# Performance work log

Hardware: AMD Instinct MI355X
Metric: run time of the kernel (lower is better)

## Reference

```python
import jax, jax.numpy as jnp
import numpy as np
from jax import lax

CIN, COUT, NCLS = 512, 256, 1
B, H, W = 4, 64, 64
EPS = 1e-5


def conv1x1(x, w):
    # x: [B,I,H,W], w: [O,I]
    return jnp.einsum('oi,bihw->bohw', w, x)


def conv3x3(x, w):
    # x: [B,I,H,W], w: [O,I,3,3], padding=1
    return lax.conv_general_dilated(x, w, (1, 1), 'SAME',
                                    dimension_numbers=('NCHW', 'OIHW', 'NCHW'))


def bn_relu(x, g, b):
    # training-mode BatchNorm2d (biased var over B,H,W) + ReLU
    mean = jnp.mean(x, axis=(0, 2, 3), keepdims=True)
    var = jnp.var(x, axis=(0, 2, 3), keepdims=True)
    xn = (x - mean) * lax.rsqrt(var + EPS)
    return jax.nn.relu(xn * g[None, :, None, None] + b[None, :, None, None])


def attention(xf, yf, wq, wk, wv, gamma):
    # cross-attn when yf != xf, self-attn when yf is xf; no 1/sqrt(d) scaling (faithful)
    Bb, C, Hh, Ww = xf.shape
    N = Hh * Ww
    q = conv1x1(xf, wq).reshape(Bb, C, N)
    k = conv1x1(yf, wk).reshape(Bb, C, N)
    v = conv1x1(yf, wv).reshape(Bb, C, N)
    att = jax.nn.softmax(jnp.einsum('bcn,bcm->bnm', q, k), axis=-1)  # [B,N,N]
    out = jnp.einsum('bcm,bnm->bcn', v, att).reshape(Bb, C, Hh, Ww)  # v @ att^T
    return gamma * out + xf


def setup_inputs() -> dict:
    key = jax.random.key(0)
    ks = jax.random.split(key, 16)
    Cs = COUT + 2

    def w(k, shape, fan_in):
        return jax.random.normal(k, shape, dtype=jnp.float32) / np.sqrt(fan_in)

    return {
        'x': jax.random.normal(ks[0], (B, CIN, H, W), dtype=jnp.float32),
        'y': jax.random.normal(ks[1], (B, CIN, H, W), dtype=jnp.float32),
        'flow': jax.random.normal(ks[2], (B, 2, H, W), dtype=jnp.float32),
        'w1x1': w(ks[3], (COUT, CIN), CIN),
        'b1x1': jnp.zeros((COUT,), dtype=jnp.float32),
        'ca_wq': w(ks[4], (COUT, COUT), COUT),
        'ca_wk': w(ks[5], (COUT, COUT), COUT),
        'ca_wv': w(ks[6], (COUT, COUT), COUT),
        'ca_gamma': jnp.full((1,), 0.1, dtype=jnp.float32),
        'cbr1_w': w(ks[7], (COUT, COUT, 3, 3), COUT * 9),
        'bn1_g': jnp.ones((COUT,), dtype=jnp.float32),
        'bn1_b': jnp.zeros((COUT,), dtype=jnp.float32),
        'sa_wq': w(ks[8], (Cs, Cs), Cs),
        'sa_wk': w(ks[9], (Cs, Cs), Cs),
        'sa_wv': w(ks[10], (Cs, Cs), Cs),
        'sa_gamma': jnp.full((1,), 0.1, dtype=jnp.float32),
        'cbr2_w': w(ks[11], (COUT, Cs, 3, 3), Cs * 9),
        'bn2_g': jnp.ones((COUT,), dtype=jnp.float32),
        'bn2_b': jnp.zeros((COUT,), dtype=jnp.float32),
        'pred_w': w(ks[12], (NCLS, COUT), COUT),
        'pred_b': jnp.zeros((NCLS,), dtype=jnp.float32),
    }


def reference(x, y, flow, w1x1, b1x1, ca_wq, ca_wk, ca_wv, ca_gamma,
              cbr1_w, bn1_g, bn1_b, sa_wq, sa_wk, sa_wv, sa_gamma,
              cbr2_w, bn2_g, bn2_b, pred_w, pred_b):
    xb = conv1x1(x, w1x1) + b1x1[None, :, None, None]
    yb = conv1x1(y, w1x1) + b1x1[None, :, None, None]
    t = attention(xb, yb, ca_wq, ca_wk, ca_wv, ca_gamma)
    cross_out = bn_relu(conv3x3(t, cbr1_w), bn1_g, bn1_b)
    cat = jnp.concatenate([cross_out, flow], axis=1)  # [B, COUT+2, H, W]
    t = attention(cat, cat, sa_wq, sa_wk, sa_wv, sa_gamma)
    t = bn_relu(conv3x3(t, cbr2_w), bn2_g, bn2_b)
    out = conv1x1(t, pred_w) + pred_b[None, :, None, None]
    return out
```

## Files before the change

### kernel.cpp

```cpp
#include <hip/hip_runtime.h>
#include <hip/hip_bf16.h>
#include <math.h>


#define NPIX 4096
#define NB   4

typedef __attribute__((ext_vector_type(8))) short short8v;
typedef __attribute__((ext_vector_type(4))) float float4v;

__device__ __forceinline__ short f2bs(float f) {
  __hip_bfloat16 h = __float2bfloat16(f);
  short r; __builtin_memcpy(&r, &h, 2); return r;
}

__global__ __launch_bounds__(256) void transp_kernel(
    const float* __restrict__ X, __hip_bfloat16* __restrict__ XT)
{
  const int i0 = blockIdx.x * 64, n0 = blockIdx.y * 64, b = blockIdx.z;
  const int tid = threadIdx.x;
  __shared__ float Ls[64][68];
#pragma unroll
  for (int it = 0; it < 4; ++it) {
    int ir = it * 16 + (tid >> 4);
    int nc = (tid & 15) * 4;
    float4 v = *(const float4*)(X + ((size_t)b * 512 + i0 + ir) * NPIX + n0 + nc);
    *(float4*)(&Ls[ir][nc]) = v;
  }
  __syncthreads();
#pragma unroll
  for (int ot = 0; ot < 2; ++ot) {
    int n = ot * 32 + (tid >> 3);
    int ig = tid & 7;
    short8v o;
#pragma unroll
    for (int j = 0; j < 8; ++j) o[j] = f2bs(Ls[8 * ig + j][n]);
    *(short8v*)(XT + ((size_t)b * NPIX + n0 + n) * 512 + i0 + 8 * ig) = o;
  }
}

__global__ void wprep_kernel(const float* __restrict__ Win,
                             __hip_bfloat16* __restrict__ Wout,
                             int Or, int Ir, int Op, int Ip)
{
  size_t total = (size_t)Op * Ip;
  for (size_t e = (size_t)blockIdx.x * 256 + threadIdx.x; e < total;
       e += (size_t)gridDim.x * 256) {
    int i = (int)(e % Ip);
    int o = (int)(e / Ip);
    float v = (o < Or && i < Ir) ? Win[(size_t)o * Ir + i] : 0.f;
    Wout[e] = __float2bfloat16(v);
  }
}

__global__ void wtransbf_kernel(const float* __restrict__ Win,
                                __hip_bfloat16* __restrict__ Wout,
                                int O, int Ir, int Ip)
{
  size_t total = (size_t)9 * O * Ip;
  for (size_t e = (size_t)blockIdx.x * 256 + threadIdx.x; e < total;
       e += (size_t)gridDim.x * 256) {
    int i = (int)(e % Ip);
    size_t r = e / Ip;
    int o = (int)(r % O);
    int dydx = (int)(r / O);
    float v = (i < Ir) ? Win[((size_t)o * Ir + i) * 9 + dydx] : 0.f;
    Wout[e] = __float2bfloat16(v);
  }
}

template<int OMODE>
__global__ __launch_bounds__(256, 3) void gemm3_kernel(
    const __hip_bfloat16* __restrict__ X, const __hip_bfloat16* __restrict__ Wb,
    const float* __restrict__ Bias, float* __restrict__ Yf,
    __hip_bfloat16* __restrict__ Yb, int Ip, int O)
{
  const int n0 = blockIdx.x * 64, o0 = blockIdx.y * 64, b = blockIdx.z;
  const int tid = threadIdx.x, wv = tid >> 6, lane = tid & 63;
  const int lg = lane >> 4, lr = lane & 15;
  __shared__ __align__(16) __hip_bfloat16 Xs[64 * 32];
  __shared__ __align__(16) __hip_bfloat16 Wsh[64 * 32];

  const int nn = tid >> 2, ig = tid & 3;
  const __hip_bfloat16* xrow = X + ((size_t)b * NPIX + n0 + nn) * Ip;
  const __hip_bfloat16* wrow = Wb + (size_t)(o0 + nn) * Ip;
  const int sw = 8 * (ig ^ (nn & 3));

  float4v acc[4];
#pragma unroll
  for (int f = 0; f < 4; ++f) acc[f] = (float4v){0.f, 0.f, 0.f, 0.f};

  const int nch = Ip >> 5;
  short8v xr_ = *(const short8v*)(xrow + sw);
  short8v wr_ = *(const short8v*)(wrow + sw);

  for (int ci = 0; ci < nch; ++ci) {
    __syncthreads();
    *(short8v*)(Xs  + nn * 32 + ig * 8) = xr_;
    *(short8v*)(Wsh + nn * 32 + ig * 8) = wr_;
    __syncthreads();
    if (ci + 1 < nch) {
      xr_ = *(const short8v*)(xrow + (ci + 1) * 32 + sw);
      wr_ = *(const short8v*)(wrow + (ci + 1) * 32 + sw);
    }
    if (OMODE < 2) {
      int ar = 16 * wv + lr;
      short8v a = *(const short8v*)(Xs + ar * 32 + 8 * (lg ^ (ar & 3)));
#pragma unroll
      for (int of = 0; of < 4; ++of) {
        int br = 16 * of + lr;
        short8v bb = *(const short8v*)(Wsh + br * 32 + 8 * (lg ^ (br & 3)));
        acc[of] = __builtin_amdgcn_mfma_f32_16x16x32_bf16(a, bb, acc[of], 0, 0, 0);
      }
    } else {
      int ar = 16 * wv + lr;
      short8v a = *(const short8v*)(Wsh + ar * 32 + 8 * (lg ^ (ar & 3)));
#pragma unroll
      for (int nf = 0; nf < 4; ++nf) {
        int br = 16 * nf + lr;
        short8v bb = *(const short8v*)(Xs + br * 32 + 8 * (lg ^ (br & 3)));
        acc[nf] = __builtin_amdgcn_mfma_f32_16x16x32_bf16(a, bb, acc[nf], 0, 0, 0);
      }
    }
  }

  if (OMODE < 2) {
#pragma unroll
    for (int r = 0; r < 4; ++r) {
      size_t row = (size_t)b * NPIX + n0 + 16 * wv + 4 * lg + r;
#pragma unroll
      for (int of = 0; of < 4; ++of) {
        int o = o0 + 16 * of + lr;
        if (o < O) {
          float v = acc[of][r] + (Bias ? Bias[o] : 0.f);
          if (OMODE == 0) Yf[row * O + o] = v;
          Yb[row * O + o] = __float2bfloat16(v);
        }
      }
    }
  } else {
#pragma unroll
    for (int r = 0; r < 4; ++r) {
      int c = o0 + 16 * wv + 4 * lg + r;
      if (c < O) {
#pragma unroll
        for (int nf = 0; nf < 4; ++nf) {
          int n = n0 + 16 * nf + lr;
          Yb[((size_t)b * O + c) * NPIX + n] = __float2bfloat16(acc[nf][r]);
        }
      }
    }
  }
}

template<int C>
__global__ __launch_bounds__(256, 2) void flash3_kernel(
    const __hip_bfloat16* __restrict__ Q, const __hip_bfloat16* __restrict__ K,
    const __hip_bfloat16* __restrict__ V,
    __hip_bfloat16* __restrict__ Opart, float* __restrict__ ml)
{
  constexpr int N = NPIX;
  constexpr int NC32 = C / 32;
  constexpr int NCF  = C / 16;
  constexpr int SPR  = C / 8;
  constexpr int NST  = C / 32;
  const int n0 = blockIdx.x * 64;
  const int split = blockIdx.y;
  const int b = blockIdx.z;
  const int tid = threadIdx.x, w = tid >> 6, lane = tid & 63;
  const int lg = lane >> 4, lr = lane & 15;

  __shared__ __align__(16) __hip_bfloat16 Ks[64 * C];
  __shared__ __align__(16) __hip_bfloat16 Vs[C * 64];
  __shared__ __align__(16) __hip_bfloat16 Ps[4][64][16];

  short8v qf[NC32];
  {
    const __hip_bfloat16* qp = Q + ((size_t)b * N + n0 + 16 * w + lr) * C + 8 * lg;
#pragma unroll
    for (int ks = 0; ks < NC32; ++ks) qf[ks] = *(const short8v*)(qp + 32 * ks);
  }

  float4v oacc[NCF];
#pragma unroll
  for (int f = 0; f < NCF; ++f) oacc[f] = (float4v){0.f, 0.f, 0.f, 0.f};
  float mrun[4], lrun[4];
#pragma unroll
  for (int r = 0; r < 4; ++r) { mrun[r] = -INFINITY; lrun[r] = 0.f; }

  const __hip_bfloat16* Kb = K + (size_t)b * N * C;
  const __hip_bfloat16* Vb = V + (size_t)b * C * N;
  const int m0 = split * (N / 2);

  short8v kreg[NST], vreg[NST];
#pragma unroll
  for (int i = 0; i < NST; ++i) {
    int s = tid + i * 256;
    int row = s / SPR, c8i = s % SPR;
    kreg[i] = *(const short8v*)(Kb + (size_t)(m0 + row) * C + 8 * (c8i ^ (row & 3)));
  }
#pragma unroll
  for (int i = 0; i < NST; ++i) {
    int s = tid + i * 256;
    int c = s >> 3, m8i = s & 7;
    vreg[i] = *(const short8v*)(Vb + (size_t)c * N + m0 + 8 * (m8i ^ (c & 3)));
  }

  for (int t = 0; t < 32; ++t) {
    __syncthreads();
#pragma unroll
    for (int i = 0; i < NST; ++i) {
      int s = tid + i * 256;
      *(short8v*)(Ks + s * 8) = kreg[i];
      *(short8v*)(Vs + s * 8) = vreg[i];
    }
    __syncthreads();
    if (t < 31) {
      const int mn = m0 + (t + 1) * 64;
#pragma unroll
      for (int i = 0; i < NST; ++i) {
        int s = tid + i * 256;
        int row = s / SPR, c8i = s % SPR;
        kreg[i] = *(const short8v*)(Kb + (size_t)(mn + row) * C + 8 * (c8i ^ (row & 3)));
      }
#pragma unroll
      for (int i = 0; i < NST; ++i) {
        int s = tid + i * 256;
        int c = s >> 3, m8i = s & 7;
        vreg[i] = *(const short8v*)(Vb + (size_t)c * N + mn + 8 * (m8i ^ (c & 3)));
      }
    }
    float4v sacc[4];
#pragma unroll
    for (int mf = 0; mf < 4; ++mf) sacc[mf] = (float4v){0.f, 0.f, 0.f, 0.f};
#pragma unroll
    for (int ks = 0; ks < NC32; ++ks)
#pragma unroll
      for (int mf = 0; mf < 4; ++mf) {
        int m = 16 * mf + lr;
        short8v k8 = *(const short8v*)(Ks + m * C + 32 * ks + 8 * (lg ^ (m & 3)));
        sacc[mf] = __builtin_amdgcn_mfma_f32_16x16x32_bf16(qf[ks], k8, sacc[mf], 0, 0, 0);
      }
    float scal[4];
#pragma unroll
    for (int r = 0; r < 4; ++r) {
      float pm = fmaxf(fmaxf(sacc[0][r], sacc[1][r]), fmaxf(sacc[2][r], sacc[3][r]));
#pragma unroll
      for (int off = 1; off < 16; off <<= 1) pm = fmaxf(pm, __shfl_xor(pm, off));
      float mnew = fmaxf(mrun[r], pm);
      float sc = __expf(mrun[r] - mnew);
      mrun[r] = mnew;
      float rs = 0.f, p[4];
#pragma unroll
      for (int mf = 0; mf < 4; ++mf) { p[mf] = __expf(sacc[mf][r] - mnew); rs += p[mf]; }
#pragma unroll
      for (int mf = 0; mf < 4; ++mf)
        Ps[mf][16 * w + 4 * lg + r][lr] = __float2bfloat16(p[mf]);
#pragma unroll
      for (int off = 1; off < 16; off <<= 1) rs += __shfl_xor(rs, off);
      lrun[r] = lrun[r] * sc + rs;
      scal[r] = sc;
    }
#pragma unroll
    for (int f = 0; f < NCF; ++f)
#pragma unroll
      for (int r = 0; r < 4; ++r) oacc[f][r] *= scal[r];

    asm volatile("s_waitcnt lgkmcnt(0)" ::: "memory");

    short8v pa0 = *(const short8v*)(&Ps[lg >> 1][16 * w + lr][8 * (lg & 1)]);
    short8v pa1 = *(const short8v*)(&Ps[2 + (lg >> 1)][16 * w + lr][8 * (lg & 1)]);
#pragma unroll
    for (int cf = 0; cf < NCF; ++cf) {
      int c = 16 * cf + lr;
      const __hip_bfloat16* vb = Vs + c * 64;
      short8v v0 = *(const short8v*)(vb + 8 * (lg ^ (c & 3)));
      short8v v1 = *(const short8v*)(vb + 32 + 8 * (lg ^ (c & 3)));
      oacc[cf] = __builtin_amdgcn_mfma_f32_16x16x32_bf16(pa0, v0, oacc[cf], 0, 0, 0);
      oacc[cf] = __builtin_amdgcn_mfma_f32_16x16x32_bf16(pa1, v1, oacc[cf], 0, 0, 0);
    }
  }
  const size_t rbase = (size_t)(split * NB + b) * N;
#pragma unroll
  for (int r = 0; r < 4; ++r) {
    int n = n0 + 16 * w + 4 * lg + r;
    if (lr == 0) { ml[(rbase + n) * 2] = mrun[r]; ml[(rbase + n) * 2 + 1] = lrun[r]; }
#pragma unroll
    for (int cf = 0; cf < NCF; ++cf)
      Opart[(rbase + n) * C + 16 * cf + lr] = __float2bfloat16(oacc[cf][r]);
  }
}

template<int C>
__global__ __launch_bounds__(256) void merge3_kernel(
    const __hip_bfloat16* __restrict__ Op, const float* __restrict__ ml,
    const float* __restrict__ R, const float* __restrict__ gamma_p,
    __hip_bfloat16* __restrict__ T)
{
  const size_t row = blockIdx.x;
  const size_t row1 = row + (size_t)NB * NPIX;
  float m0 = ml[row * 2],  l0 = ml[row * 2 + 1];
  float m1 = ml[row1 * 2], l1 = ml[row1 * 2 + 1];
  float m = fmaxf(m0, m1);
  float e0 = __expf(m0 - m), e1 = __expf(m1 - m);
  float rinv = gamma_p[0] / (l0 * e0 + l1 * e1);
  for (int c = threadIdx.x; c < C; c += 256) {
    float o = __bfloat162float(Op[row * C + c]) * e0 +
              __bfloat162float(Op[row1 * C + c]) * e1;
    T[row * C + c] = __float2bfloat16(o * rinv + R[row * C + c]);
  }
}

template<int IC>
__global__ __launch_bounds__(256, 2) void conv3_kernel(
    const __hip_bfloat16* __restrict__ X, const __hip_bfloat16* __restrict__ W2,
    float* __restrict__ Y)
{
  constexpr int NCH = IC / 32;
  constexpr int XP = 66 * 32;
  const int h = blockIdx.x, o0 = blockIdx.y * 64, b = blockIdx.z;
  const int tid = threadIdx.x, wv = tid >> 6, lane = tid & 63;
  const int lg = lane >> 4, lr = lane & 15;

  __shared__ __align__(16) __hip_bfloat16 Ws[9 * 64 * 32];
  __shared__ __align__(16) __hip_bfloat16 X3[3 * XP];

  for (int e = tid; e < 192; e += 256) {
    int p = e / 64, rr = (e >> 5) & 1, i = e & 31;
    X3[p * XP + (rr ? 65 * 32 : 0) + i] = __float2bfloat16(0.f);
  }

  float4v acc[4];
#pragma unroll
  for (int f = 0; f < 4; ++f) acc[f] = (float4v){0.f, 0.f, 0.f, 0.f};

  short8v xreg[3], wreg[9];
#define LOADX(CI)                                                              \
  _Pragma("unroll")                                                            \
  for (int j = 0; j < 3; ++j) {                                                \
    int s = tid + j * 256;                                                     \
    int dy = s >> 8, ww = (s >> 2) & 63, ig = s & 3;                           \
    int hs = h + dy - 1;                                                       \
    if (hs >= 0 && hs < 64)                                                    \
      xreg[j] = *(const short8v*)(X + ((size_t)b * NPIX + hs * 64 + ww) * IC + \
                                  (CI) * 32 + 8 * (ig ^ ((ww + 1) & 3)));      \
    else                                                                       \
      xreg[j] = (short8v){0, 0, 0, 0, 0, 0, 0, 0};                             \
  }
#define LOADW(CI)                                                              \
  _Pragma("unroll")                                                            \
  for (int j = 0; j < 9; ++j) {                                                \
    int s = tid + j * 256;                                                     \
    int dydx = s >> 8, oo = (s >> 2) & 63, ig = s & 3;                         \
    wreg[j] = *(const short8v*)(W2 + ((size_t)(dydx * 256 + o0 + oo)) * IC +   \
                                (CI) * 32 + 8 * (ig ^ (oo & 3)));              \
  }
  LOADX(0); LOADW(0);

  for (int ci = 0; ci < NCH; ++ci) {
    __syncthreads();
#pragma unroll
    for (int j = 0; j < 3; ++j) {
      int s = tid + j * 256;
      int dy = s >> 8, ww = (s >> 2) & 63, ig = s & 3;
      *(short8v*)(X3 + dy * XP + (ww + 1) * 32 + ig * 8) = xreg[j];
    }
#pragma unroll
    for (int j = 0; j < 9; ++j) {
      int s = tid + j * 256;
      *(short8v*)(Ws + s * 8) = wreg[j];
    }
    __syncthreads();
    if (ci + 1 < NCH) { LOADX(ci + 1); LOADW(ci + 1); }
#pragma unroll
    for (int dy = 0; dy < 3; ++dy)
#pragma unroll
      for (int dx = 0; dx < 3; ++dx) {
        int rs_ = 16 * wv + lr + dx;
        short8v a = *(const short8v*)(X3 + dy * XP + rs_ * 32 + 8 * (lg ^ (rs_ & 3)));
#pragma unroll
        for (int of = 0; of < 4; ++of) {
          int br = 16 * of + lr;
          short8v bb = *(const short8v*)(Ws + (dy * 3 + dx) * 2048 + br * 32 +
                                         8 * (lg ^ (br & 3)));
          acc[of] = __builtin_amdgcn_mfma_f32_16x16x32_bf16(a, bb, acc[of], 0, 0, 0);
        }
      }
  }
#pragma unroll
  for (int r = 0; r < 4; ++r) {
    size_t row = (size_t)b * NPIX + h * 64 + 16 * wv + 4 * lg + r;
#pragma unroll
    for (int of = 0; of < 4; ++of)
      Y[row * 256 + o0 + 16 * of + lr] = acc[of][r];
  }
#undef LOADX
#undef LOADW
}

__global__ __launch_bounds__(256) void stats1_kernel(
    const float* __restrict__ X, float* __restrict__ Part)
{
  const int o0 = (blockIdx.x & 3) * 64;
  const int rc = blockIdx.x >> 2;
  const int tid = threadIdx.x;
  const int o = o0 + (tid & 63), rq = tid >> 6;
  float s = 0.f, sq = 0.f;
  for (int rr = rq; rr < 256; rr += 4) {
    float v = X[(size_t)(rc * 256 + rr) * 256 + o];
    s += v; sq += v * v;
  }
  __shared__ float rs[256], rq2[256];
  rs[tid] = s; rq2[tid] = sq;
  __syncthreads();
  if (tid < 64) {
    s  = rs[tid] + rs[tid + 64] + rs[tid + 128] + rs[tid + 192];
    sq = rq2[tid] + rq2[tid + 64] + rq2[tid + 128] + rq2[tid + 192];
    Part[(o0 + tid) * 128 + rc * 2]     = s;
    Part[(o0 + tid) * 128 + rc * 2 + 1] = sq;
  }
}

__global__ __launch_bounds__(256) void stats2_kernel(
    const float* __restrict__ Part, float* __restrict__ Mean, float* __restrict__ Rstd)
{
  const int o = threadIdx.x;
  float s = 0.f, sq = 0.f;
  for (int rc = 0; rc < 64; ++rc) {
    s += Part[o * 128 + rc * 2];
    sq += Part[o * 128 + rc * 2 + 1];
  }
  float mean = s / 16384.f;
  float var = sq / 16384.f - mean * mean;
  Mean[o] = mean;
  Rstd[o] = 1.f / sqrtf(var + 1e-5f);
}

__global__ __launch_bounds__(320) void bnapply1_kernel(
    const float* __restrict__ X, const float* __restrict__ Flow,
    const float* __restrict__ Mean, const float* __restrict__ Rstd,
    const float* __restrict__ G, const float* __restrict__ Bt,
    float* __restrict__ CatF, __hip_bfloat16* __restrict__ CatB)
{
  const size_t row = blockIdx.x;
  const int t = threadIdx.x;
  if (t >= 288) return;
  float val;
  if (t < 256) {
    float v = X[row * 256 + t];
    val = fmaxf((v - Mean[t]) * Rstd[t] * G[t] + Bt[t], 0.f);
  } else if (t < 258) {
    int b = (int)(row >> 12), n = (int)(row & 4095);
    val = Flow[((size_t)(b * 2 + (t - 256)) << 12) + n];
  } else val = 0.f;
  CatF[row * 288 + t] = val;
  CatB[row * 288 + t] = __float2bfloat16(val);
}

__global__ __launch_bounds__(256) void bnapply2_kernel(
    float* X, const float* __restrict__ Mean, const float* __restrict__ Rstd,
    const float* __restrict__ G, const float* __restrict__ Bt)
{
  const size_t idx = (size_t)blockIdx.x * 256 + threadIdx.x;
  const int t = threadIdx.x;
  float v = X[idx];
  X[idx] = fmaxf((v - Mean[t]) * Rstd[t] * G[t] + Bt[t], 0.f);
}

__global__ __launch_bounds__(256) void pred3_kernel(
    const float* __restrict__ X, const float* __restrict__ Wp,
    const float* __restrict__ Bp, float* __restrict__ Out)
{
  const int wv = threadIdx.x >> 6, lane = threadIdx.x & 63;
  const size_t row = (size_t)blockIdx.x * 4 + wv;
  const float* xr = X + row * 256;
  float acc = 0.f;
#pragma unroll
  for (int cc = 0; cc < 4; ++cc) acc = fmaf(xr[cc * 64 + lane], Wp[cc * 64 + lane], acc);
#pragma unroll
  for (int off = 1; off < 64; off <<= 1) acc += __shfl_xor(acc, off);
  if (lane == 0) Out[row] = acc + Bp[0];
}

extern "C" void kernel_launch(void* const* d_in, const int* in_sizes, int n_in,
                              void* d_out, int out_size, void* d_ws, size_t ws_size,
                              hipStream_t stream)
{
  (void)in_sizes; (void)n_in; (void)out_size; (void)ws_size;
  const float* x      = (const float*)d_in[0];
  const float* y      = (const float*)d_in[1];
  const float* flow   = (const float*)d_in[2];
  const float* w1x1   = (const float*)d_in[3];
  const float* b1x1   = (const float*)d_in[4];
  const float* ca_wq  = (const float*)d_in[5];
  const float* ca_wk  = (const float*)d_in[6];
  const float* ca_wv  = (const float*)d_in[7];
  const float* ca_g   = (const float*)d_in[8];
  const float* cbr1_w = (const float*)d_in[9];
  const float* bn1_g  = (const float*)d_in[10];
  const float* bn1_b  = (const float*)d_in[11];
  const float* sa_wq  = (const float*)d_in[12];
  const float* sa_wk  = (const float*)d_in[13];
  const float* sa_wv  = (const float*)d_in[14];
  const float* sa_g   = (const float*)d_in[15];
  const float* cbr2_w = (const float*)d_in[16];
  const float* bn2_g  = (const float*)d_in[17];
  const float* bn2_b  = (const float*)d_in[18];
  const float* pred_w = (const float*)d_in[19];
  const float* pred_b = (const float*)d_in[20];
  float* out = (float*)d_out;

  const size_t FSZ = (size_t)NB * NPIX * 288;
  const size_t SSZ = FSZ / 2;
  float* ws = (float*)d_ws;
  float* F0 = ws;
  float* F1 = ws + FSZ;
  float* F2 = ws + 2 * FSZ;
  float* Sb = ws + 3 * FSZ;
  __hip_bfloat16* S0 = (__hip_bfloat16*)(Sb);
  __hip_bfloat16* S1 = (__hip_bfloat16*)(Sb + SSZ);
  __hip_bfloat16* S2 = (__hip_bfloat16*)(Sb + 2 * SSZ);
  __hip_bfloat16* S3 = (__hip_bfloat16*)(Sb + 3 * SSZ);
  __hip_bfloat16* S4 = (__hip_bfloat16*)(Sb + 4 * SSZ);
  float* Wr = Sb + 5 * SSZ;
  __hip_bfloat16* w1bf  = (__hip_bfloat16*)Wr;
  __hip_bfloat16* caqb  = w1bf + (size_t)256 * 512;
  __hip_bfloat16* cakb  = caqb + (size_t)256 * 256;
  __hip_bfloat16* cavb  = cakb + (size_t)256 * 256;
  __hip_bfloat16* saqb  = cavb + (size_t)256 * 256;
  __hip_bfloat16* sakb  = saqb + (size_t)320 * 288;
  __hip_bfloat16* savb  = sakb + (size_t)320 * 288;
  __hip_bfloat16* w2abf = savb + (size_t)320 * 288;
  __hip_bfloat16* w2bbf = w2abf + (size_t)9 * 256 * 256;
  float* Part = (float*)(w2bbf + (size_t)9 * 256 * 288);
  float* Mean = Part + 32768;
  float* Rstd = Mean + 256;
  float* Mlb  = Rstd + 256;

  __hip_bfloat16* xT = (__hip_bfloat16*)F0;
  __hip_bfloat16* yT = (__hip_bfloat16*)F1;
  __hip_bfloat16* Op = (__hip_bfloat16*)F0;

  dim3 blk(256);

  wprep_kernel<<<dim3(256), blk, 0, stream>>>(w1x1, w1bf, 256, 512, 256, 512);
  wprep_kernel<<<dim3(256), blk, 0, stream>>>(ca_wq, caqb, 256, 256, 256, 256);
  wprep_kernel<<<dim3(256), blk, 0, stream>>>(ca_wk, cakb, 256, 256, 256, 256);
  wprep_kernel<<<dim3(256), blk, 0, stream>>>(ca_wv, cavb, 256, 256, 256, 256);
  wprep_kernel<<<dim3(256), blk, 0, stream>>>(sa_wq, saqb, 258, 258, 320, 288);
  wprep_kernel<<<dim3(256), blk, 0, stream>>>(sa_wk, sakb, 258, 258, 320, 288);
  wprep_kernel<<<dim3(256), blk, 0, stream>>>(sa_wv, savb, 258, 258, 320, 288);
  wtransbf_kernel<<<dim3(512), blk, 0, stream>>>(cbr1_w, w2abf, 256, 256, 256);
  wtransbf_kernel<<<dim3(512), blk, 0, stream>>>(cbr2_w, w2bbf, 256, 258, 288);

  transp_kernel<<<dim3(8, 64, 4), blk, 0, stream>>>(x, xT);
  transp_kernel<<<dim3(8, 64, 4), blk, 0, stream>>>(y, yT);

  gemm3_kernel<0><<<dim3(64, 4, 4), blk, 0, stream>>>(xT, w1bf, b1x1, F2, S0, 512, 256);
  gemm3_kernel<1><<<dim3(64, 4, 4), blk, 0, stream>>>(yT, w1bf, b1x1, nullptr, S1, 512, 256);

  gemm3_kernel<1><<<dim3(64, 4, 4), blk, 0, stream>>>(S0, caqb, nullptr, nullptr, S2, 256, 256);
  gemm3_kernel<1><<<dim3(64, 4, 4), blk, 0, stream>>>(S1, cakb, nullptr, nullptr, S3, 256, 256);
  gemm3_kernel<2><<<dim3(64, 4, 4), blk, 0, stream>>>(S1, cavb, nullptr, nullptr, S4, 256, 256);

  flash3_kernel<256><<<dim3(64, 2, 4), blk, 0, stream>>>(S2, S3, S4, Op, Mlb);
  merge3_kernel<256><<<dim3(16384), blk, 0, stream>>>(Op, Mlb, F2, ca_g, S0);

  conv3_kernel<256><<<dim3(64, 4, 4), blk, 0, stream>>>(S0, w2abf, F0);
  stats1_kernel<<<dim3(256), blk, 0, stream>>>(F0, Part);
  stats2_kernel<<<dim3(1), blk, 0, stream>>>(Part, Mean, Rstd);
  bnapply1_kernel<<<dim3(16384), dim3(320), 0, stream>>>(F0, flow, Mean, Rstd,
                                                         bn1_g, bn1_b, F1, S3);

  gemm3_kernel<1><<<dim3(64, 5, 4), blk, 0, stream>>>(S3, saqb, nullptr, nullptr, S0, 288, 288);
  gemm3_kernel<1><<<dim3(64, 5, 4), blk, 0, stream>>>(S3, sakb, nullptr, nullptr, S1, 288, 288);
  gemm3_kernel<2><<<dim3(64, 5, 4), blk, 0, stream>>>(S3, savb, nullptr, nullptr, S2, 288, 288);

  flash3_kernel<288><<<dim3(64, 2, 4), blk, 0, stream>>>(S0, S1, S2, Op, Mlb);
  merge3_kernel<288><<<dim3(16384), blk, 0, stream>>>(Op, Mlb, F1, sa_g, S4);

  conv3_kernel<288><<<dim3(64, 4, 4), blk, 0, stream>>>(S4, w2bbf, F0);
  stats1_kernel<<<dim3(256), blk, 0, stream>>>(F0, Part);
  stats2_kernel<<<dim3(1), blk, 0, stream>>>(Part, Mean, Rstd);
  bnapply2_kernel<<<dim3(16384), blk, 0, stream>>>(F0, Mean, Rstd, bn2_g, bn2_b);

  pred3_kernel<<<dim3(4096), blk, 0, stream>>>(F0, pred_w, pred_b, out);
}
```

Before: 625.4 us.

## Rework flash attention with direct-to-LDS K/V loads and blocked layouts

The K and V projection GEMMs now write blocked layouts with 8-element chunks contiguous, so the attention kernel can pull tiles with global_load_lds straight into shared memory instead of staging them through registers. The new flash kernel also processes several query fragments per wave to reuse each K/V fragment, reuses the K buffer for P, raises wave priority around the MFMA loops, and uses a four-way KV split for cross attention with a generalized merge. The trade-off is that the register prefetch pipelining is lost, since each tile waits on vmcnt(0) before compute, and there are more partial outputs to merge.

Measured after the change: 545.0 us. 12.9% less time.

```diff
diff --git a/kernel.cpp b/kernel.cpp
--- a/kernel.cpp
+++ b/kernel.cpp
@@ -12,6 +12,12 @@
 __device__ __forceinline__ short f2bs(float f) {
   __hip_bfloat16 h = __float2bfloat16(f);
   short r; __builtin_memcpy(&r, &h, 2); return r;
+}
+
+__device__ __forceinline__ void glld16(const void* g, void* l) {
+  __builtin_amdgcn_global_load_lds(
+      (const __attribute__((address_space(1))) unsigned int*)g,
+      (__attribute__((address_space(3))) unsigned int*)l, 16, 0, 0);
 }
 
 __global__ __launch_bounds__(256) void transp_kernel(
@@ -103,7 +109,7 @@
       xr_ = *(const short8v*)(xrow + (ci + 1) * 32 + sw);
       wr_ = *(const short8v*)(wrow + (ci + 1) * 32 + sw);
     }
-    if (OMODE < 2) {
+    if (OMODE != 4) {
       int ar = 16 * wv + lr;
       short8v a = *(const short8v*)(Xs + ar * 32 + 8 * (lg ^ (ar & 3)));
 #pragma unroll
@@ -138,7 +144,20 @@
         }
       }
     }
+  } else if (OMODE == 3) {
+    __hip_bfloat16* Hb = Yb + (size_t)b * NPIX * O;
+#pragma unroll
+    for (int r = 0; r < 4; ++r) {
+      size_t n = n0 + 16 * wv + 4 * lg + r;
+#pragma unroll
+      for (int of = 0; of < 4; ++of) {
+        int o = o0 + 16 * of + lr;
+        if (o < O)
+          Hb[((size_t)(o >> 3) * NPIX + n) * 8 + (o & 7)] = __float2bfloat16(acc[of][r]);
+      }
+    }
   } else {
+    __hip_bfloat16* Hb = Yb + (size_t)b * NPIX * O;
 #pragma unroll
     for (int r = 0; r < 4; ++r) {
       int c = o0 + 16 * wv + 4 * lg + r;
@@ -146,167 +165,187 @@
 #pragma unroll
         for (int nf = 0; nf < 4; ++nf) {
           int n = n0 + 16 * nf + lr;
-          Yb[((size_t)b * O + c) * NPIX + n] = __float2bfloat16(acc[nf][r]);
+          Hb[((size_t)(n >> 3) * O + c) * 8 + (n & 7)] = __float2bfloat16(acc[nf][r]);
         }
       }
     }
   }
 }
 
-template<int C>
-__global__ __launch_bounds__(256, 2) void flash3_kernel(
+template<int C, int RF, int S>
+__global__ __launch_bounds__(256, 2) void flash4_kernel(
     const __hip_bfloat16* __restrict__ Q, const __hip_bfloat16* __restrict__ K,
     const __hip_bfloat16* __restrict__ V,
     __hip_bfloat16* __restrict__ Opart, float* __restrict__ ml)
 {
-  constexpr int N = NPIX;
+  constexpr int N    = NPIX;
   constexpr int NC32 = C / 32;
   constexpr int NCF  = C / 16;
-  constexpr int SPR  = C / 8;
-  constexpr int NST  = C / 32;
-  const int n0 = blockIdx.x * 64;
-  const int split = blockIdx.y;
-  const int b = blockIdx.z;
+  constexpr int QB   = 16 * RF;
+  constexpr int KBYTES = 128 * C;
+  constexpr int NT   = (N / S) / 64;
+
+  __shared__ __align__(1024) char smem[256 * C];
+  __hip_bfloat16* Ks = (__hip_bfloat16*)smem;
+  __hip_bfloat16* Vs = (__hip_bfloat16*)(smem + KBYTES);
+  __hip_bfloat16* Ps = (__hip_bfloat16*)smem;
+
+  const int n0 = blockIdx.x * (4 * QB);
+  const int split = blockIdx.y, b = blockIdx.z;
   const int tid = threadIdx.x, w = tid >> 6, lane = tid & 63;
   const int lg = lane >> 4, lr = lane & 15;
 
-  __shared__ __align__(16) __hip_bfloat16 Ks[64 * C];
-  __shared__ __align__(16) __hip_bfloat16 Vs[C * 64];
-  __shared__ __align__(16) __hip_bfloat16 Ps[4][64][16];
-
-  short8v qf[NC32];
-  {
-    const __hip_bfloat16* qp = Q + ((size_t)b * N + n0 + 16 * w + lr) * C + 8 * lg;
-#pragma unroll
-    for (int ks = 0; ks < NC32; ++ks) qf[ks] = *(const short8v*)(qp + 32 * ks);
-  }
-
-  float4v oacc[NCF];
-#pragma unroll
-  for (int f = 0; f < NCF; ++f) oacc[f] = (float4v){0.f, 0.f, 0.f, 0.f};
-  float mrun[4], lrun[4];
-#pragma unroll
-  for (int r = 0; r < 4; ++r) { mrun[r] = -INFINITY; lrun[r] = 0.f; }
-
   const __hip_bfloat16* Kb = K + (size_t)b * N * C;
-  const __hip_bfloat16* Vb = V + (size_t)b * C * N;
-  const int m0 = split * (N / 2);
-
-  short8v kreg[NST], vreg[NST];
-#pragma unroll
-  for (int i = 0; i < NST; ++i) {
-    int s = tid + i * 256;
-    int row = s / SPR, c8i = s % SPR;
-    kreg[i] = *(const short8v*)(Kb + (size_t)(m0 + row) * C + 8 * (c8i ^ (row & 3)));
-  }
-#pragma unroll
-  for (int i = 0; i < NST; ++i) {
-    int s = tid + i * 256;
-    int c = s >> 3, m8i = s & 7;
-    vreg[i] = *(const short8v*)(Vb + (size_t)c * N + m0 + 8 * (m8i ^ (c & 3)));
-  }
-
-  for (int t = 0; t < 32; ++t) {
+  const __hip_bfloat16* Vb = V + (size_t)b * N * C;
+
+  short8v qf[RF][NC32];
+#pragma unroll
+  for (int rf = 0; rf < RF; ++rf) {
+    const __hip_bfloat16* qp =
+        Q + ((size_t)b * N + n0 + QB * w + 16 * rf + lr) * C + 8 * lg;
+#pragma unroll
+    for (int ks = 0; ks < NC32; ++ks) qf[rf][ks] = *(const short8v*)(qp + 32 * ks);
+  }
+
+  float4v oacc[RF][NCF];
+#pragma unroll
+  for (int rf = 0; rf < RF; ++rf)
+#pragma unroll
+    for (int f = 0; f < NCF; ++f) oacc[rf][f] = (float4v){0.f, 0.f, 0.f, 0.f};
+  float mrun[RF][4], lrun[RF][4];
+#pragma unroll
+  for (int rf = 0; rf < RF; ++rf)
+#pragma unroll
+    for (int r = 0; r < 4; ++r) { mrun[rf][r] = -INFINITY; lrun[rf][r] = 0.f; }
+
+  const int m0base = split * (N / S);
+
+  for (int t = 0; t < NT; ++t) {
+    const int m0 = m0base + t * 64;
     __syncthreads();
-#pragma unroll
-    for (int i = 0; i < NST; ++i) {
-      int s = tid + i * 256;
-      *(short8v*)(Ks + s * 8) = kreg[i];
-      *(short8v*)(Vs + s * 8) = vreg[i];
-    }
+    for (int u = w; u < C / 8; u += 4)
+      glld16(Kb + ((size_t)u * N + m0 + lane) * 8, Ks + u * 512);
+    for (int u = w; u < C / 8; u += 4) {
+      int s = u * 64 + lane;
+      int kv8 = s / C, c = s % C;
+      glld16(Vb + ((size_t)(m0 / 8 + kv8) * C + c) * 8, Vs + u * 512);
+    }
+    asm volatile("s_waitcnt vmcnt(0)" ::: "memory");
     __syncthreads();
-    if (t < 31) {
-      const int mn = m0 + (t + 1) * 64;
-#pragma unroll
-      for (int i = 0; i < NST; ++i) {
-        int s = tid + i * 256;
-        int row = s / SPR, c8i = s % SPR;
-        kreg[i] = *(const short8v*)(Kb + (size_t)(mn + row) * C + 8 * (c8i ^ (row & 3)));
-      }
-#pragma unroll
-      for (int i = 0; i < NST; ++i) {
-        int s = tid + i * 256;
-        int c = s >> 3, m8i = s & 7;
-        vreg[i] = *(const short8v*)(Vb + (size_t)c * N + mn + 8 * (m8i ^ (c & 3)));
-      }
-    }
-    float4v sacc[4];
-#pragma unroll
-    for (int mf = 0; mf < 4; ++mf) sacc[mf] = (float4v){0.f, 0.f, 0.f, 0.f};
+
+    float4v sacc[RF][4];
+#pragma unroll
+    for (int rf = 0; rf < RF; ++rf)
+#pragma unroll
+      for (int mf = 0; mf < 4; ++mf) sacc[rf][mf] = (float4v){0.f, 0.f, 0.f, 0.f};
+    __builtin_amdgcn_s_setprio(1);
 #pragma unroll
     for (int ks = 0; ks < NC32; ++ks)
 #pragma unroll
       for (int mf = 0; mf < 4; ++mf) {
-        int m = 16 * mf + lr;
-        short8v k8 = *(const short8v*)(Ks + m * C + 32 * ks + 8 * (lg ^ (m & 3)));
-        sacc[mf] = __builtin_amdgcn_mfma_f32_16x16x32_bf16(qf[ks], k8, sacc[mf], 0, 0, 0);
-      }
-    float scal[4];
+        short8v kf = *(const short8v*)(Ks + ((4 * ks + lg) * 64 + 16 * mf + lr) * 8);
+#pragma unroll
+        for (int rf = 0; rf < RF; ++rf)
+          sacc[rf][mf] =
+              __builtin_amdgcn_mfma_f32_16x16x32_bf16(qf[rf][ks], kf, sacc[rf][mf], 0, 0, 0);
+      }
+    __builtin_amdgcn_s_setprio(0);
+    __syncthreads();
+
+    float scal[RF][4];
+#pragma unroll
+    for (int rf = 0; rf < RF; ++rf)
+#pragma unroll
+      for (int r = 0; r < 4; ++r) {
+        float pm = fmaxf(fmaxf(sacc[rf][0][r], sacc[rf][1][r]),
+                         fmaxf(sacc[rf][2][r], sacc[rf][3][r]));
+#pragma unroll
+        for (int off = 1; off < 16; off <<= 1) pm = fmaxf(pm, __shfl_xor(pm, off));
+        float mnew = fmaxf(mrun[rf][r], pm);
+        float sc = __expf(mrun[rf][r] - mnew);
+        mrun[rf][r] = mnew;
+        float rs = 0.f;
+#pragma unroll
+        for (int mf = 0; mf < 4; ++mf) {
+          float p = __expf(sacc[rf][mf][r] - mnew);
+          rs += p;
+          Ps[(size_t)(w * QB + 16 * rf + 4 * lg + r) * 72 + 16 * mf + lr] =
+              __float2bfloat16(p);
+        }
+#pragma unroll
+        for (int off = 1; off < 16; off <<= 1) rs += __shfl_xor(rs, off);
+        lrun[rf][r] = lrun[rf][r] * sc + rs;
+        scal[rf][r] = sc;
+      }
+#pragma unroll
+    for (int rf = 0; rf < RF; ++rf)
+#pragma unroll
+      for (int f = 0; f < NCF; ++f)
+#pragma unroll
+        for (int r = 0; r < 4; ++r) oacc[rf][f][r] *= scal[rf][r];
+
+    asm volatile("s_waitcnt lgkmcnt(0)" ::: "memory");
+
+    short8v pa[RF][2];
+#pragma unroll
+    for (int rf = 0; rf < RF; ++rf)
+#pragma unroll
+      for (int h = 0; h < 2; ++h)
+        pa[rf][h] = *(const short8v*)(Ps + (size_t)(w * QB + 16 * rf + lr) * 72 +
+                                      32 * h + 8 * lg);
+    __builtin_amdgcn_s_setprio(1);
+#pragma unroll
+    for (int cf = 0; cf < NCF; ++cf)
+#pragma unroll
+      for (int h = 0; h < 2; ++h) {
+        short8v vf = *(const short8v*)(Vs + ((h * 4 + lg) * C + 16 * cf + lr) * 8);
+#pragma unroll
+        for (int rf = 0; rf < RF; ++rf)
+          oacc[rf][cf] =
+              __builtin_amdgcn_mfma_f32_16x16x32_bf16(pa[rf][h], vf, oacc[rf][cf], 0, 0, 0);
+      }
+    __builtin_amdgcn_s_setprio(0);
+  }
+
+  const size_t rbase = (size_t)(split * NB + b) * N;
+#pragma unroll
+  for (int rf = 0; rf < RF; ++rf)
 #pragma unroll
     for (int r = 0; r < 4; ++r) {
-      float pm = fmaxf(fmaxf(sacc[0][r], sacc[1][r]), fmaxf(sacc[2][r], sacc[3][r]));
-#pragma unroll
-      for (int off = 1; off < 16; off <<= 1) pm = fmaxf(pm, __shfl_xor(pm, off));
-      float mnew = fmaxf(mrun[r], pm);
-      float sc = __expf(mrun[r] - mnew);
-      mrun[r] = mnew;
-      float rs = 0.f, p[4];
-#pragma unroll
-      for (int mf = 0; mf < 4; ++mf) { p[mf] = __expf(sacc[mf][r] - mnew); rs += p[mf]; }
-#pragma unroll
-      for (int mf = 0; mf < 4; ++mf)
-        Ps[mf][16 * w + 4 * lg + r][lr] = __float2bfloat16(p[mf]);
-#pragma unroll
-      for (int off = 1; off < 16; off <<= 1) rs += __shfl_xor(rs, off);
-      lrun[r] = lrun[r] * sc + rs;
-      scal[r] = sc;
-    }
-#pragma unroll
-    for (int f = 0; f < NCF; ++f)
-#pragma unroll
-      for (int r = 0; r < 4; ++r) oacc[f][r] *= scal[r];
-
-    asm volatile("s_waitcnt lgkmcnt(0)" ::: "memory");
-
-    short8v pa0 = *(const short8v*)(&Ps[lg >> 1][16 * w + lr][8 * (lg & 1)]);
-    short8v pa1 = *(const short8v*)(&Ps[2 + (lg >> 1)][16 * w + lr][8 * (lg & 1)]);
-#pragma unroll
-    for (int cf = 0; cf < NCF; ++cf) {
-      int c = 16 * cf + lr;
-      const __hip_bfloat16* vb = Vs + c * 64;
-      short8v v0 = *(const short8v*)(vb + 8 * (lg ^ (c & 3)));
-      short8v v1 = *(const short8v*)(vb + 32 + 8 * (lg ^ (c & 3)));
-      oacc[cf] = __builtin_amdgcn_mfma_f32_16x16x32_bf16(pa0, v0, oacc[cf], 0, 0, 0);
-      oacc[cf] = __builtin_amdgcn_mfma_f32_16x16x32_bf16(pa1, v1, oacc[cf], 0, 0, 0);
-    }
-  }
-  const size_t rbase = (size_t)(split * NB + b) * N;
-#pragma unroll
-  for (int r = 0; r < 4; ++r) {
-    int n = n0 + 16 * w + 4 * lg + r;
-    if (lr == 0) { ml[(rbase + n) * 2] = mrun[r]; ml[(rbase + n) * 2 + 1] = lrun[r]; }
-#pragma unroll
-    for (int cf = 0; cf < NCF; ++cf)
-      Opart[(rbase + n) * C + 16 * cf + lr] = __float2bfloat16(oacc[cf][r]);
-  }
-}
-
-template<int C>
-__global__ __launch_bounds__(256) void merge3_kernel(
+      int n = n0 + QB * w + 16 * rf + 4 * lg + r;
+      if (lr == 0) {
+        ml[(rbase + n) * 2]     = mrun[rf][r];
+        ml[(rbase + n) * 2 + 1] = lrun[rf][r];
+      }
+#pragma unroll
+      for (int cf = 0; cf < NCF; ++cf)
+        Opart[(rbase + n) * C + 16 * cf + lr] = __float2bfloat16(oacc[rf][cf][r]);
+    }
+}
+
+template<int C, int S>
+__global__ __launch_bounds__(256) void merge4_kernel(
     const __hip_bfloat16* __restrict__ Op, const float* __restrict__ ml,
     const float* __restrict__ R, const float* __restrict__ gamma_p,
     __hip_bfloat16* __restrict__ T)
 {
   const size_t row = blockIdx.x;
-  const size_t row1 = row + (size_t)NB * NPIX;
-  float m0 = ml[row * 2],  l0 = ml[row * 2 + 1];
-  float m1 = ml[row1 * 2], l1 = ml[row1 * 2 + 1];
-  float m = fmaxf(m0, m1);
-  float e0 = __expf(m0 - m), e1 = __expf(m1 - m);
-  float rinv = gamma_p[0] / (l0 * e0 + l1 * e1);
+  float m = -INFINITY;
+#pragma unroll
+  for (int s = 0; s < S; ++s)
+    m = fmaxf(m, ml[((size_t)s * NB * NPIX + row) * 2]);
+  float e[S]; float L = 0.f;
+#pragma unroll
+  for (int s = 0; s < S; ++s) {
+    e[s] = __expf(ml[((size_t)s * NB * NPIX + row) * 2] - m);
+    L += ml[((size_t)s * NB * NPIX + row) * 2 + 1] * e[s];
+  }
+  float rinv = gamma_p[0] / L;
   for (int c = threadIdx.x; c < C; c += 256) {
-    float o = __bfloat162float(Op[row * C + c]) * e0 +
-              __bfloat162float(Op[row1 * C + c]) * e1;
+    float o = 0.f;
+#pragma unroll
+    for (int s = 0; s < S; ++s)
+      o += __bfloat162float(Op[((size_t)s * NB * NPIX + row) * C + c]) * e[s];
     T[row * C + c] = __float2bfloat16(o * rinv + R[row * C + c]);
   }
 }
@@ -560,11 +599,11 @@
   gemm3_kernel<1><<<dim3(64, 4, 4), blk, 0, stream>>>(yT, w1bf, b1x1, nullptr, S1, 512, 256);
 
   gemm3_kernel<1><<<dim3(64, 4, 4), blk, 0, stream>>>(S0, caqb, nullptr, nullptr, S2, 256, 256);
-  gemm3_kernel<1><<<dim3(64, 4, 4), blk, 0, stream>>>(S1, cakb, nullptr, nullptr, S3, 256, 256);
-  gemm3_kernel<2><<<dim3(64, 4, 4), blk, 0, stream>>>(S1, cavb, nullptr, nullptr, S4, 256, 256);
-
-  flash3_kernel<256><<<dim3(64, 2, 4), blk, 0, stream>>>(S2, S3, S4, Op, Mlb);
-  merge3_kernel<256><<<dim3(16384), blk, 0, stream>>>(Op, Mlb, F2, ca_g, S0);
+  gemm3_kernel<3><<<dim3(64, 4, 4), blk, 0, stream>>>(S1, cakb, nullptr, nullptr, S3, 256, 256);
+  gemm3_kernel<4><<<dim3(64, 4, 4), blk, 0, stream>>>(S1, cavb, nullptr, nullptr, S4, 256, 256);
+
+  flash4_kernel<256, 2, 4><<<dim3(32, 4, 4), blk, 0, stream>>>(S2, S3, S4, Op, Mlb);
+  merge4_kernel<256, 4><<<dim3(16384), blk, 0, stream>>>(Op, Mlb, F2, ca_g, S0);
 
   conv3_kernel<256><<<dim3(64, 4, 4), blk, 0, stream>>>(S0, w2abf, F0);
   stats1_kernel<<<dim3(256), blk, 0, stream>>>(F0, Part);
@@ -573,11 +612,11 @@
                                                          bn1_g, bn1_b, F1, S3);
 
   gemm3_kernel<1><<<dim3(64, 5, 4), blk, 0, stream>>>(S3, saqb, nullptr, nullptr, S0, 288, 288);
-  gemm3_kernel<1><<<dim3(64, 5, 4), blk, 0, stream>>>(S3, sakb, nullptr, nullptr, S1, 288, 288);
-  gemm3_kernel<2><<<dim3(64, 5, 4), blk, 0, stream>>>(S3, savb, nullptr, nullptr, S2, 288, 288);
-
-  flash3_kernel<288><<<dim3(64, 2, 4), blk, 0, stream>>>(S0, S1, S2, Op, Mlb);
-  merge3_kernel<288><<<dim3(16384), blk, 0, stream>>>(Op, Mlb, F1, sa_g, S4);
+  gemm3_kernel<3><<<dim3(64, 5, 4), blk, 0, stream>>>(S3, sakb, nullptr, nullptr, S1, 288, 288);
+  gemm3_kernel<4><<<dim3(64, 5, 4), blk, 0, stream>>>(S3, savb, nullptr, nullptr, S2, 288, 288);
+
+  flash4_kernel<288, 1, 2><<<dim3(64, 2, 4), blk, 0, stream>>>(S0, S1, S2, Op, Mlb);
+  merge4_kernel<288, 2><<<dim3(16384), blk, 0, stream>>>(Op, Mlb, F1, sa_g, S4);
 
   conv3_kernel<288><<<dim3(64, 4, 4), blk, 0, stream>>>(S4, w2bbf, F0);
   stats1_kernel<<<dim3(256), blk, 0, stream>>>(F0, Part);
```
